# Kernel tuning notes

Measured on AMD Instinct MI355X. Metric: run time of the kernel, lower is better.

## Reference

```python
import jax, jax.numpy as jnp
import numpy as np

H = 128          # hidden_dim
EPS = 1e-5       # BatchNorm eps


def _mean_aggr(h_src, src_idx, dst_idx, num_dst):
    # scatter-mean of h_src rows (gathered by src_idx) onto dst nodes
    msgs = h_src[src_idx]                                   # [E, H] gather
    s = jax.ops.segment_sum(msgs, dst_idx, num_segments=num_dst)
    c = jax.ops.segment_sum(jnp.ones((dst_idx.shape[0],), h_src.dtype),
                            dst_idx, num_segments=num_dst)
    return s / jnp.maximum(c, 1.0)[:, None]


def _bn_eval(h, g, b, m, v):
    return (h - m) * jax.lax.rsqrt(v + EPS) * g + b


def setup_inputs() -> dict:
    key = jax.random.key(0)
    ks = jax.random.split(key, 32)
    Nu, Nr, E, Din, ED = 100000, 100000, 500000, 32, 16
    d = {}
    d['x_user'] = jax.random.normal(ks[0], (Nu, Din), jnp.float32)
    d['x_recipient'] = jax.random.normal(ks[1], (Nr, Din), jnp.float32)
    d['edge_attr'] = jax.random.normal(ks[2], (E, ED), jnp.float32)
    d['edge_index_ut'] = jax.random.randint(ks[3], (2, E), 0, Nr)  # user->recipient
    d['edge_index_ru'] = jax.random.randint(ks[4], (2, E), 0, Nu)  # recipient->user
    sc = 0.05
    # input projections (Linear: y = x @ W + b, W stored [in, out])
    d['proj_uW'] = jax.random.normal(ks[5], (Din, H), jnp.float32) * sc
    d['proj_ub'] = jnp.zeros((H,), jnp.float32)
    d['proj_rW'] = jax.random.normal(ks[6], (Din, H), jnp.float32) * sc
    d['proj_rb'] = jnp.zeros((H,), jnp.float32)
    # SAGEConv params: [num_layers=2, num_edge_types=2, ...]
    d['sage_Wl'] = jax.random.normal(ks[7], (2, 2, H, H), jnp.float32) * sc
    d['sage_bl'] = jnp.zeros((2, 2, H), jnp.float32)
    d['sage_Wr'] = jax.random.normal(ks[8], (2, 2, H, H), jnp.float32) * sc
    # BatchNorm (eval): [num_layers=2, num_node_types=2 (0=user,1=recipient), H]
    d['bn_g'] = jnp.ones((2, 2, H), jnp.float32)
    d['bn_b'] = jnp.zeros((2, 2, H), jnp.float32)
    d['bn_m'] = jax.random.normal(ks[9], (2, 2, H), jnp.float32) * 0.01
    d['bn_v'] = jnp.ones((2, 2, H), jnp.float32)
    # EdgePredictor MLP: (2H + edge_dim) -> H -> H//2 -> 1
    din = 2 * H + ED
    d['ep_W1'] = jax.random.normal(ks[10], (din, H), jnp.float32) * sc
    d['ep_b1'] = jnp.zeros((H,), jnp.float32)
    d['ep_bng'] = jnp.ones((H,), jnp.float32)
    d['ep_bnb'] = jnp.zeros((H,), jnp.float32)
    d['ep_bnm'] = jax.random.normal(ks[11], (H,), jnp.float32) * 0.01
    d['ep_bnv'] = jnp.ones((H,), jnp.float32)
    d['ep_W2'] = jax.random.normal(ks[12], (H, H // 2), jnp.float32) * sc
    d['ep_b2'] = jnp.zeros((H // 2,), jnp.float32)
    d['ep_W3'] = jax.random.normal(ks[13], (H // 2, 1), jnp.float32) * sc
    d['ep_b3'] = jnp.zeros((1,), jnp.float32)
    return d


def reference(x_user, x_recipient, edge_attr, edge_index_ut, edge_index_ru,
              proj_uW, proj_ub, proj_rW, proj_rb,
              sage_Wl, sage_bl, sage_Wr,
              bn_g, bn_b, bn_m, bn_v,
              ep_W1, ep_b1, ep_bng, ep_bnb, ep_bnm, ep_bnv,
              ep_W2, ep_b2, ep_W3, ep_b3):
    Nu = x_user.shape[0]
    Nr = x_recipient.shape[0]
    # input projections
    h_u = x_user @ proj_uW + proj_ub        # [Nu, H]
    h_r = x_recipient @ proj_rW + proj_rb   # [Nr, H]

    for i in range(2):  # num_layers
        # edge type 0: user -> recipient (SAGE mean aggr + root)
        agg_r = _mean_aggr(h_u, edge_index_ut[0], edge_index_ut[1], Nr)
        new_r = agg_r @ sage_Wl[i, 0] + sage_bl[i, 0] + h_r @ sage_Wr[i, 0]
        # edge type 1: recipient -> user
        agg_u = _mean_aggr(h_r, edge_index_ru[0], edge_index_ru[1], Nu)
        new_u = agg_u @ sage_Wl[i, 1] + sage_bl[i, 1] + h_u @ sage_Wr[i, 1]
        # BN (eval) + ReLU (dropout inactive) + residual
        new_u = jax.nn.relu(_bn_eval(new_u, bn_g[i, 0], bn_b[i, 0], bn_m[i, 0], bn_v[i, 0])) + h_u
        new_r = jax.nn.relu(_bn_eval(new_r, bn_g[i, 1], bn_b[i, 1], bn_m[i, 1], bn_v[i, 1])) + h_r
        h_u, h_r = new_u, new_r

    # edge predictor on target edge type (user -> recipient)
    src = h_u[edge_index_ut[0]]   # [E, H]
    dst = h_r[edge_index_ut[1]]   # [E, H]
    x = jnp.concatenate([src, dst, edge_attr], axis=1)  # [E, 2H+ED]
    h = jax.nn.relu(x @ ep_W1 + ep_b1)
    h = _bn_eval(h, ep_bng, ep_bnb, ep_bnm, ep_bnv)
    h = jax.nn.relu(h @ ep_W2 + ep_b2)
    out = jax.nn.sigmoid(h @ ep_W3 + ep_b3)
    return out.squeeze(-1)  # [E]
```

## Files before the change

### kernel.cpp

```cpp
#include <hip/hip_runtime.h>
#include <math.h>

#define H 128
#define BN_EPS 1e-5f

typedef __attribute__((ext_vector_type(8))) short bf16x8;
typedef __attribute__((ext_vector_type(4))) float f32x4;

__device__ __forceinline__ unsigned short f2bf(float f) {
    unsigned int u = __float_as_uint(f);
    u += 0x7fffu + ((u >> 16) & 1u);
    return (unsigned short)(u >> 16);
}
__device__ __forceinline__ float bf2f(unsigned short s) {
    return __uint_as_float(((unsigned int)s) << 16);
}
__device__ __forceinline__ f32x4 mfma16(bf16x8 a, bf16x8 b, f32x4 c) {
    return __builtin_amdgcn_mfma_f32_16x16x32_bf16(a, b, c, 0, 0, 0);
}

__device__ __forceinline__ void wfrag_one(const float* __restrict__ src,
                                          unsigned short* __restrict__ dst,
                                          int K, int N, int idx) {
    int l = idx & 63;
    int rest = idx >> 6;
    int ntn = N >> 4;
    int nt = rest % ntn;
    int kc = rest / ntn;
    int n = nt * 16 + (l & 15);
    int k0 = kc * 32 + (l >> 4) * 8;
    bf16x8 v;
    #pragma unroll
    for (int j = 0; j < 8; ++j) {
        int k = k0 + j;
        v[j] = (short)((k < K) ? f2bf(src[(size_t)k * N + n]) : 0);
    }
    *(bf16x8*)(dst + (size_t)idx * 8) = v;
}

__global__ __launch_bounds__(256)
void wfrag_all(const float* __restrict__ W1, const float* __restrict__ W2,
               const float* __restrict__ pu, const float* __restrict__ pr,
               const float* __restrict__ Wl, const float* __restrict__ Wr,
               unsigned short* __restrict__ W1f, unsigned short* __restrict__ W2f,
               unsigned short* __restrict__ puf, unsigned short* __restrict__ prf,
               unsigned short* __restrict__ sageWf) {
    int bx = blockIdx.x;
    if (bx < 26) {
        int idx = bx * 256 + threadIdx.x;
        if (idx < 4608)      wfrag_one(W1, W1f, 272, 128, idx);
        else if (idx < 5632) wfrag_one(W2, W2f, 128, 64, idx - 4608);
        else if (idx < 6144) wfrag_one(pu, puf, 32, 128, idx - 5632);
        else if (idx < 6656) wfrag_one(pr, prf, 32, 128, idx - 6144);
    } else {
        int idx = (bx - 26) * 256 + threadIdx.x;
        int seg = idx >> 11;
        int sub = idx & 2047;
        int lt = seg >> 1;
        int half = seg & 1;
        const float* src = (half ? Wr : Wl) + (size_t)lt * H * H;
        unsigned short* dst = sageWf + (size_t)lt * 32768 + half * 16384;
        wfrag_one(src, dst, 128, 128, sub);
    }
}

__global__ __launch_bounds__(256)
void proj_kernel(const float* __restrict__ xu, const float* __restrict__ xr,
                 const unsigned short* __restrict__ puf, const float* __restrict__ bu,
                 const unsigned short* __restrict__ prf, const float* __restrict__ br,
                 unsigned short* __restrict__ hub, unsigned short* __restrict__ hrb,
                 int Nu, int Nr, int nbu) {
    int bx = blockIdx.x;
    const float* x; const unsigned short* Wf; const float* bias;
    unsigned short* hb; int N; int row0;
    if (bx < nbu) { x = xu; Wf = puf; bias = bu; hb = hub; N = Nu; row0 = bx * 64; }
    else          { x = xr; Wf = prf; bias = br; hb = hrb; N = Nr; row0 = (bx - nbu) * 64; }

    int tid = threadIdx.x, l = tid & 63, w = tid >> 6, l15 = l & 15, quad = l >> 4;
    int arow = row0 + w * 16 + l15;

    bf16x8 a = {0, 0, 0, 0, 0, 0, 0, 0};
    if (arow < N) {
        const float* xp = x + (size_t)arow * 32 + quad * 8;
        float4 v0 = *(const float4*)xp;
        float4 v1 = *(const float4*)(xp + 4);
        a[0] = (short)f2bf(v0.x); a[1] = (short)f2bf(v0.y);
        a[2] = (short)f2bf(v0.z); a[3] = (short)f2bf(v0.w);
        a[4] = (short)f2bf(v1.x); a[5] = (short)f2bf(v1.y);
        a[6] = (short)f2bf(v1.z); a[7] = (short)f2bf(v1.w);
    }
    f32x4 acc[8];
    #pragma unroll
    for (int nt = 0; nt < 8; ++nt) {
        bf16x8 b = *(const bf16x8*)(Wf + (size_t)(nt * 64 + l) * 8);
        acc[nt] = mfma16(a, b, (f32x4){0.f, 0.f, 0.f, 0.f});
    }
    #pragma unroll
    for (int reg = 0; reg < 4; ++reg) {
        int row = row0 + w * 16 + quad * 4 + reg;
        if (row < N) {
            #pragma unroll
            for (int nt = 0; nt < 8; ++nt) {
                int col = nt * 16 + l15;
                hb[(size_t)row * H + col] = f2bf(acc[nt][reg] + bias[col]);
            }
        }
    }
}

__global__ __launch_bounds__(256)
void hist_kernel(const int* __restrict__ dstR, const int* __restrict__ dstU,
                 int* __restrict__ degR, int* __restrict__ degU, int E, int EB) {
    int bx = blockIdx.x;
    const int* dst = (bx < EB) ? dstR : dstU;
    int* deg = (bx < EB) ? degR : degU;
    int e = ((bx < EB) ? bx : bx - EB) * 256 + threadIdx.x;
    if (e < E) atomicAdd(&deg[dst[e]], 1);
}

__global__ __launch_bounds__(256)
void scan1_kernel(const int* __restrict__ degR, const int* __restrict__ degU,
                  int* __restrict__ partR, int* __restrict__ partU, int Nr, int Nu, int NBr) {
    int bx = blockIdx.x;
    const int* deg = (bx < NBr) ? degR : degU;
    int* part = (bx < NBr) ? partR : partU;
    int lb = (bx < NBr) ? bx : bx - NBr;
    int N = (bx < NBr) ? Nr : Nu;
    __shared__ int s[256];
    int t = threadIdx.x;
    int i = lb * 256 + t;
    s[t] = (i < N) ? deg[i] : 0;
    __syncthreads();
    for (int o = 128; o > 0; o >>= 1) {
        if (t < o) s[t] += s[t + o];
        __syncthreads();
    }
    if (t == 0) part[lb] = s[0];
}

__global__ __launch_bounds__(256)
void scan3_kernel(const int* __restrict__ degR, const int* __restrict__ degU,
                  const int* __restrict__ partR, const int* __restrict__ partU,
                  int* __restrict__ offR, int* __restrict__ offU, int Nr, int Nu, int NBr) {
    int bx = blockIdx.x;
    const int* deg = (bx < NBr) ? degR : degU;
    const int* part = (bx < NBr) ? partR : partU;
    int* off = (bx < NBr) ? offR : offU;
    int lb = (bx < NBr) ? bx : bx - NBr;
    int N = (bx < NBr) ? Nr : Nu;
    __shared__ int s[256];
    __shared__ int ps[256];
    int t = threadIdx.x;

    int pv = 0;
    if (t < lb) pv += part[t];
    if (t + 256 < lb) pv += part[t + 256];
    ps[t] = pv;
    __syncthreads();
    for (int o = 128; o > 0; o >>= 1) {
        if (t < o) ps[t] += ps[t + o];
        __syncthreads();
    }
    int pref = ps[0];

    int i = lb * 256 + t;
    int v = (i < N) ? deg[i] : 0;
    s[t] = v;
    __syncthreads();
    for (int o = 1; o < 256; o <<= 1) {
        int x = (t >= o) ? s[t - o] : 0;
        __syncthreads();
        s[t] += x;
        __syncthreads();
    }
    if (i < N) off[i] = pref + s[t] - v;
    if (i == N - 1) off[N] = pref + s[t];
}

__global__ __launch_bounds__(256)
void fill_kernel(const int* __restrict__ srcR, const int* __restrict__ dstR,
                 const int* __restrict__ srcU, const int* __restrict__ dstU,
                 const int* __restrict__ offR, const int* __restrict__ offU,
                 int* __restrict__ degR, int* __restrict__ degU,
                 int* __restrict__ eidR, int* __restrict__ eidU,
                 int* __restrict__ epermR, int* __restrict__ epdstR,
                 int E, int EB) {
    int bx = blockIdx.x;
    bool isR = bx < EB;
    const int* src = isR ? srcR : srcU;
    const int* dst = isR ? dstR : dstU;
    const int* off = isR ? offR : offU;
    int* deg = isR ? degR : degU;
    int* eid = isR ? eidR : eidU;
    int e = (isR ? bx : bx - EB) * 256 + threadIdx.x;
    if (e < E) {
        int d = dst[e];
        int p = off[d] + atomicSub(&deg[d], 1) - 1;
        eid[p] = src[e];
        if (isR) {
            epermR[p] = e;
            epdstR[p] = d;
        }
    }
}

__global__ __launch_bounds__(256)
void layer_kernel(const unsigned short* __restrict__ hu_o, const unsigned short* __restrict__ hr_o,
                  unsigned short* __restrict__ hu_n, unsigned short* __restrict__ hr_n,
                  const int* __restrict__ off_r, const int* __restrict__ eid_r,
                  const int* __restrict__ off_u, const int* __restrict__ eid_u,
                  int Nu, int Nr, int nbr,
                  const unsigned short* __restrict__ WfR, const float* __restrict__ blR,
                  const float* __restrict__ gR, const float* __restrict__ bR,
                  const float* __restrict__ mR, const float* __restrict__ vR,
                  const unsigned short* __restrict__ WfU, const float* __restrict__ blU,
                  const float* __restrict__ gU, const float* __restrict__ bU,
                  const float* __restrict__ mU, const float* __restrict__ vU) {
    int bx = blockIdx.x;
    const unsigned short* gsrc; const unsigned short* own; unsigned short* outp;
    const int* off; const int* eid; const unsigned short* Wf;
    const float *bl, *bg, *bb, *bm, *bv;
    int N, row0;
    if (bx < nbr) {
        gsrc = hu_o; own = hr_o; outp = hr_n; off = off_r; eid = eid_r;
        Wf = WfR; bl = blR; bg = gR; bb = bR; bm = mR; bv = vR;
        N = Nr; row0 = bx * 64;
    } else {
        gsrc = hr_o; own = hu_o; outp = hu_n; off = off_u; eid = eid_u;
        Wf = WfU; bl = blU; bg = gU; bb = bU; bm = mU; bv = vU;
        N = Nu; row0 = (bx - nbr) * 64;
    }

    __shared__ float sc[128], sh[128], bias[128];
    __shared__ int perm[64];
    int tid = threadIdx.x;
    if (tid < 128) {
        float s = bg[tid] * rsqrtf(bv[tid] + BN_EPS);
        sc[tid] = s;
        sh[tid] = bb[tid] - bm[tid] * s;
        bias[tid] = bl[tid];
    }
    if (tid < 64) {
        int rr = row0 + tid;
        int dg = (rr < N) ? (off[rr + 1] - off[rr]) : 0;
        int key = (min(dg, 255) << 8) | tid;
        for (int k = 2; k <= 64; k <<= 1) {
            for (int j = k >> 1; j > 0; j >>= 1) {
                int p = __shfl_xor(key, j);
                bool keepmin = (((tid & j) == 0) == ((tid & k) == 0));
                key = keepmin ? (key < p ? key : p) : (key > p ? key : p);
            }
        }
        perm[tid] = key & 255;
    }
    __syncthreads();

    int l = tid & 63, w = tid >> 6, l15 = l & 15, quad = l >> 4;
    int rloc = perm[w * 16 + l15];
    int arow = row0 + rloc;
    bool rok = (arow < N);
    size_t rbase = (size_t)(rok ? arow : 0) * H;
    int s0 = rok ? off[arow] : 0;
    int s1 = rok ? off[arow + 1] : 0;

    bf16x8 ownfr[4];
    #pragma unroll
    for (int kc = 0; kc < 4; ++kc)
        ownfr[kc] = *(const bf16x8*)(own + rbase + kc * 32 + quad * 8);

    float ag[4][8];
    #pragma unroll
    for (int kc = 0; kc < 4; ++kc)
        #pragma unroll
        for (int j = 0; j < 8; ++j) ag[kc][j] = 0.0f;

    for (int i = s0; i < s1; ++i) {
        int s = eid[i];
        const unsigned short* rp = gsrc + (size_t)s * H + quad * 8;
        #pragma unroll
        for (int kc = 0; kc < 4; ++kc) {
            bf16x8 v = *(const bf16x8*)(rp + kc * 32);
            #pragma unroll
            for (int j = 0; j < 8; ++j) ag[kc][j] += bf2f((unsigned short)v[j]);
        }
    }
    float inv = (s1 > s0) ? 1.0f / (float)(s1 - s0) : 0.0f;

    f32x4 acc[8];
    #pragma unroll
    for (int nt = 0; nt < 8; ++nt) acc[nt] = (f32x4){0.f, 0.f, 0.f, 0.f};

    #pragma unroll
    for (int kc = 0; kc < 4; ++kc) {
        bf16x8 a;
        #pragma unroll
        for (int j = 0; j < 8; ++j) a[j] = (short)f2bf(ag[kc][j] * inv);
        #pragma unroll
        for (int nt = 0; nt < 8; ++nt) {
            bf16x8 b = *(const bf16x8*)(Wf + (size_t)((kc * 8 + nt) * 64 + l) * 8);
            acc[nt] = mfma16(a, b, acc[nt]);
        }
    }
    #pragma unroll
    for (int kc = 4; kc < 8; ++kc) {
        #pragma unroll
        for (int nt = 0; nt < 8; ++nt) {
            bf16x8 b = *(const bf16x8*)(Wf + (size_t)((kc * 8 + nt) * 64 + l) * 8);
            acc[nt] = mfma16(ownfr[kc - 4], b, acc[nt]);
        }
    }

    #pragma unroll
    for (int reg = 0; reg < 4; ++reg) {
        int crow = row0 + perm[w * 16 + quad * 4 + reg];
        if (crow < N) {
            #pragma unroll
            for (int nt = 0; nt < 8; ++nt) {
                int col = nt * 16 + l15;
                float g = acc[nt][reg] + bias[col];
                g = g * sc[col] + sh[col];
                float hv = bf2f(own[(size_t)crow * H + col]);
                outp[(size_t)crow * H + col] = f2bf(fmaxf(g, 0.0f) + hv);
            }
        }
    }
}

__global__ __launch_bounds__(256)
void ep_kernel(const unsigned short* __restrict__ hub, const unsigned short* __restrict__ hrb,
               const float* __restrict__ ea,
               const int* __restrict__ slot_src, const int* __restrict__ slot_dst,
               const int* __restrict__ slot_eid,
               const unsigned short* __restrict__ W1f, const float* __restrict__ b1,
               const float* __restrict__ bng, const float* __restrict__ bnb,
               const float* __restrict__ bnm, const float* __restrict__ bnv,
               const unsigned short* __restrict__ W2f, const float* __restrict__ b2,
               const float* __restrict__ W3, const float* __restrict__ b3,
               float* __restrict__ out, int E) {
    __shared__ unsigned short h1s[64][136];
    __shared__ int se[64], de[64], pe[64];
    __shared__ float sc1[128], sh1[128], bi1[128];

    int tid = threadIdx.x;
    int p0 = blockIdx.x * 64;
    if (tid < 64) {
        int p = p0 + tid;
        bool v = (p < E);
        se[tid] = v ? slot_src[p] : 0;
        de[tid] = v ? slot_dst[p] : 0;
        pe[tid] = v ? slot_eid[p] : 0;
    }
    if (tid < 128) {
        float s = bng[tid] * rsqrtf(bnv[tid] + BN_EPS);
        sc1[tid] = s;
        sh1[tid] = bnb[tid] - bnm[tid] * s;
        bi1[tid] = b1[tid];
    }
    __syncthreads();

    int l = tid & 63, w = tid >> 6, l15 = l & 15, quad = l >> 4;
    int arow = w * 16 + l15;
    size_t soff = (size_t)se[arow] * H;
    size_t doff = (size_t)de[arow] * H;
    int eorig = pe[arow];
    bool ev = (p0 + arow < E);

    bf16x8 afr[9];
    #pragma unroll
    for (int kc = 0; kc < 4; ++kc)
        afr[kc] = *(const bf16x8*)(hub + soff + kc * 32 + quad * 8);
    #pragma unroll
    for (int kc = 0; kc < 4; ++kc)
        afr[4 + kc] = *(const bf16x8*)(hrb + doff + kc * 32 + quad * 8);
    {
        bf16x8 a = {0, 0, 0, 0, 0, 0, 0, 0};
        if (quad < 2 && ev) {
            const float* p = ea + (size_t)eorig * 16 + quad * 8;
            float4 v0 = *(const float4*)p;
            float4 v1 = *(const float4*)(p + 4);
            a[0] = (short)f2bf(v0.x); a[1] = (short)f2bf(v0.y);
            a[2] = (short)f2bf(v0.z); a[3] = (short)f2bf(v0.w);
            a[4] = (short)f2bf(v1.x); a[5] = (short)f2bf(v1.y);
            a[6] = (short)f2bf(v1.z); a[7] = (short)f2bf(v1.w);
        }
        afr[8] = a;
    }

    f32x4 acc[8];
    #pragma unroll
    for (int nt = 0; nt < 8; ++nt) acc[nt] = (f32x4){0.f, 0.f, 0.f, 0.f};

    #pragma unroll
    for (int kc = 0; kc < 9; ++kc) {
        #pragma unroll
        for (int nt = 0; nt < 8; ++nt) {
            bf16x8 b = *(const bf16x8*)(W1f + (size_t)((kc * 8 + nt) * 64 + l) * 8);
            acc[nt] = mfma16(afr[kc], b, acc[nt]);
        }
    }

    #pragma unroll
    for (int nt = 0; nt < 8; ++nt) {
        #pragma unroll
        for (int reg = 0; reg < 4; ++reg) {
            int row = w * 16 + quad * 4 + reg;
            int col = nt * 16 + l15;
            float z = acc[nt][reg] + bi1[col];
            z = fmaxf(z, 0.0f);
            z = z * sc1[col] + sh1[col];
            h1s[row][col] = f2bf(z);
        }
    }
    __syncthreads();

    f32x4 acc2[4];
    #pragma unroll
    for (int nt = 0; nt < 4; ++nt) acc2[nt] = (f32x4){0.f, 0.f, 0.f, 0.f};
    #pragma unroll
    for (int kc = 0; kc < 4; ++kc) {
        bf16x8 a2 = *(const bf16x8*)&h1s[w * 16 + l15][kc * 32 + quad * 8];
        #pragma unroll
        for (int nt = 0; nt < 4; ++nt) {
            bf16x8 b = *(const bf16x8*)(W2f + (size_t)((kc * 4 + nt) * 64 + l) * 8);
            acc2[nt] = mfma16(a2, b, acc2[nt]);
        }
    }

    float part[4] = {0.f, 0.f, 0.f, 0.f};
    #pragma unroll
    for (int nt = 0; nt < 4; ++nt) {
        int col = nt * 16 + l15;
        float w3v = W3[col];
        float b2v = b2[col];
        #pragma unroll
        for (int reg = 0; reg < 4; ++reg)
            part[reg] += fmaxf(acc2[nt][reg] + b2v, 0.0f) * w3v;
    }
    #pragma unroll
    for (int m = 1; m < 16; m <<= 1) {
        #pragma unroll
        for (int reg = 0; reg < 4; ++reg)
            part[reg] += __shfl_xor(part[reg], m);
    }
    if (l15 < 4) {
        int row = w * 16 + quad * 4 + l15;
        if (p0 + row < E) {
            int eo = pe[row];
            out[eo] = 1.0f / (1.0f + expf(-(part[l15] + b3[0])));
        }
    }
}

extern "C" void kernel_launch(void* const* d_in, const int* in_sizes, int n_in,
                              void* d_out, int out_size, void* d_ws, size_t ws_size,
                              hipStream_t stream) {
    const float* x_u     = (const float*)d_in[0];
    const float* x_r     = (const float*)d_in[1];
    const float* eattr   = (const float*)d_in[2];
    const int*   ei_ut   = (const int*)d_in[3];
    const int*   ei_ru   = (const int*)d_in[4];
    const float* proj_uW = (const float*)d_in[5];
    const float* proj_ub = (const float*)d_in[6];
    const float* proj_rW = (const float*)d_in[7];
    const float* proj_rb = (const float*)d_in[8];
    const float* sage_Wl = (const float*)d_in[9];
    const float* sage_bl = (const float*)d_in[10];
    const float* sage_Wr = (const float*)d_in[11];
    const float* bn_g    = (const float*)d_in[12];
    const float* bn_b    = (const float*)d_in[13];
    const float* bn_m    = (const float*)d_in[14];
    const float* bn_v    = (const float*)d_in[15];
    const float* ep_W1   = (const float*)d_in[16];
    const float* ep_b1   = (const float*)d_in[17];
    const float* ep_bng  = (const float*)d_in[18];
    const float* ep_bnb  = (const float*)d_in[19];
    const float* ep_bnm  = (const float*)d_in[20];
    const float* ep_bnv  = (const float*)d_in[21];
    const float* ep_W2   = (const float*)d_in[22];
    const float* ep_b2   = (const float*)d_in[23];
    const float* ep_W3   = (const float*)d_in[24];
    const float* ep_b3   = (const float*)d_in[25];

    int Nu = in_sizes[0] / 32;
    int Nr = in_sizes[1] / 32;
    int E  = in_sizes[3] / 2;

    unsigned short* us = (unsigned short*)d_ws;
    unsigned short* h0_u = us;   us += (size_t)Nu * H;
    unsigned short* h0_r = us;   us += (size_t)Nr * H;
    unsigned short* h1_u = us;   us += (size_t)Nu * H;
    unsigned short* h1_r = us;   us += (size_t)Nr * H;
    unsigned short* W1f  = us;   us += 36864;
    unsigned short* W2f  = us;   us += 8192;
    unsigned short* puf  = us;   us += 4096;
    unsigned short* prf  = us;   us += 4096;
    unsigned short* sageWf = us; us += 131072;
    int* ip     = (int*)us;
    int* off_r  = ip;  ip += Nr + 1;
    int* off_u  = ip;  ip += Nu + 1;
    int* deg_r  = ip;  ip += Nr;
    int* deg_u  = ip;  ip += Nu;
    int* eid_r  = ip;  ip += E;
    int* eid_u  = ip;  ip += E;
    int* eperm_r = ip; ip += E;
    int* epdst_r = ip; ip += E;
    int* part_r = ip;  ip += 512;
    int* part_u = ip;  ip += 512;

    const int* ut_src = ei_ut;
    const int* ut_dst = ei_ut + E;
    const int* ru_src = ei_ru;
    const int* ru_dst = ei_ru + E;

    int EB  = (E + 255) / 256;
    int NBr = (Nr + 255) / 256;
    int NBu = (Nu + 255) / 256;

    wfrag_all<<<90, 256, 0, stream>>>(ep_W1, ep_W2, proj_uW, proj_rW,
                                      sage_Wl, sage_Wr,
                                      W1f, W2f, puf, prf, sageWf);

    hipMemsetAsync(deg_r, 0, (size_t)(Nr + Nu) * sizeof(int), stream);
    hist_kernel<<<2 * EB, 256, 0, stream>>>(ut_dst, ru_dst, deg_r, deg_u, E, EB);
    scan1_kernel<<<NBr + NBu, 256, 0, stream>>>(deg_r, deg_u, part_r, part_u, Nr, Nu, NBr);
    scan3_kernel<<<NBr + NBu, 256, 0, stream>>>(deg_r, deg_u, part_r, part_u,
                                                off_r, off_u, Nr, Nu, NBr);
    fill_kernel<<<2 * EB, 256, 0, stream>>>(ut_src, ut_dst, ru_src, ru_dst,
                                            off_r, off_u, deg_r, deg_u,
                                            eid_r, eid_u, eperm_r, epdst_r, E, EB);

    int nbu = (Nu + 63) / 64, nbr = (Nr + 63) / 64;
    proj_kernel<<<nbu + nbr, 256, 0, stream>>>(x_u, x_r, puf, proj_ub, prf, proj_rb,
                                               h0_u, h0_r, Nu, Nr, nbu);

    for (int layer = 0; layer < 2; ++layer) {
        const unsigned short* iu = (layer == 0) ? h0_u : h1_u;
        const unsigned short* ir = (layer == 0) ? h0_r : h1_r;
        unsigned short* ou = (layer == 0) ? h1_u : h0_u;
        unsigned short* orr = (layer == 0) ? h1_r : h0_r;

        const unsigned short* Wf0 = sageWf + ((size_t)layer * 2 + 0) * 32768;
        const unsigned short* Wf1 = sageWf + ((size_t)layer * 2 + 1) * 32768;
        const float* bl0 = sage_bl + ((size_t)layer * 2 + 0) * H;
        const float* bl1 = sage_bl + ((size_t)layer * 2 + 1) * H;
        const float* g0 = bn_g + ((size_t)layer * 2 + 0) * H;
        const float* b0 = bn_b + ((size_t)layer * 2 + 0) * H;
        const float* m0 = bn_m + ((size_t)layer * 2 + 0) * H;
        const float* v0 = bn_v + ((size_t)layer * 2 + 0) * H;
        const float* g1 = bn_g + ((size_t)layer * 2 + 1) * H;
        const float* b1 = bn_b + ((size_t)layer * 2 + 1) * H;
        const float* m1 = bn_m + ((size_t)layer * 2 + 1) * H;
        const float* v1 = bn_v + ((size_t)layer * 2 + 1) * H;

        layer_kernel<<<nbr + nbu, 256, 0, stream>>>(
            iu, ir, ou, orr,
            off_r, eid_r, off_u, eid_u,
            Nu, Nr, nbr,
            Wf0, bl0, g1, b1, m1, v1,
            Wf1, bl1, g0, b0, m0, v0);
    }

    ep_kernel<<<(E + 63) / 64, 256, 0, stream>>>(h0_u, h0_r, eattr,
                                                 eid_r, epdst_r, eperm_r,
                                                 W1f, ep_b1,
                                                 ep_bng, ep_bnb, ep_bnm, ep_bnv,
                                                 W2f, ep_b2, ep_W3, ep_b3,
                                                 (float*)d_out, E);
}
```

Baseline: 553.8 us.

## Keep an FP8 shadow copy of node features for gathers in layers and edge predictor

Proj and layer kernels now also write an FP8 (swizzled) copy of each node's hidden vector next to the bf16 one. The mean-aggregation gathers and the edge-predictor gathers read these 128-byte FP8 rows instead of 256-byte bf16 rows, cutting random-gather traffic in half. This costs an extra scattered byte store per element, conversion work, and a large loss of precision in the aggregated messages and edge-predictor inputs.

```diff
diff --git a/kernel.cpp b/kernel.cpp
--- a/kernel.cpp
+++ b/kernel.cpp
@@ -6,6 +6,7 @@
 
 typedef __attribute__((ext_vector_type(8))) short bf16x8;
 typedef __attribute__((ext_vector_type(4))) float f32x4;
+typedef __attribute__((ext_vector_type(2))) float f32x2;
 
 __device__ __forceinline__ unsigned short f2bf(float f) {
     unsigned int u = __float_as_uint(f);
@@ -17,6 +18,10 @@
 }
 __device__ __forceinline__ f32x4 mfma16(bf16x8 a, bf16x8 b, f32x4 c) {
     return __builtin_amdgcn_mfma_f32_16x16x32_bf16(a, b, c, 0, 0, 0);
+}
+__device__ __forceinline__ unsigned char f2fp8(float f) {
+    int p = __builtin_amdgcn_cvt_pk_fp8_f32(f, f, 0, false);
+    return (unsigned char)(p & 0xff);
 }
 
 __device__ __forceinline__ void wfrag_one(const float* __restrict__ src,
@@ -64,17 +69,25 @@
     }
 }
 
+__device__ __forceinline__ int swz_of(int col) {
+    int kc = col >> 5;
+    int q = (col >> 3) & 3;
+    int j = col & 7;
+    return q * 32 + kc * 8 + j;
+}
+
 __global__ __launch_bounds__(256)
 void proj_kernel(const float* __restrict__ xu, const float* __restrict__ xr,
                  const unsigned short* __restrict__ puf, const float* __restrict__ bu,
                  const unsigned short* __restrict__ prf, const float* __restrict__ br,
                  unsigned short* __restrict__ hub, unsigned short* __restrict__ hrb,
+                 unsigned char* __restrict__ h8u, unsigned char* __restrict__ h8r,
                  int Nu, int Nr, int nbu) {
     int bx = blockIdx.x;
     const float* x; const unsigned short* Wf; const float* bias;
-    unsigned short* hb; int N; int row0;
-    if (bx < nbu) { x = xu; Wf = puf; bias = bu; hb = hub; N = Nu; row0 = bx * 64; }
-    else          { x = xr; Wf = prf; bias = br; hb = hrb; N = Nr; row0 = (bx - nbu) * 64; }
+    unsigned short* hb; unsigned char* h8; int N; int row0;
+    if (bx < nbu) { x = xu; Wf = puf; bias = bu; hb = hub; h8 = h8u; N = Nu; row0 = bx * 64; }
+    else          { x = xr; Wf = prf; bias = br; hb = hrb; h8 = h8r; N = Nr; row0 = (bx - nbu) * 64; }
 
     int tid = threadIdx.x, l = tid & 63, w = tid >> 6, l15 = l & 15, quad = l >> 4;
     int arow = row0 + w * 16 + l15;
@@ -102,7 +115,9 @@
             #pragma unroll
             for (int nt = 0; nt < 8; ++nt) {
                 int col = nt * 16 + l15;
-                hb[(size_t)row * H + col] = f2bf(acc[nt][reg] + bias[col]);
+                float v = acc[nt][reg] + bias[col];
+                hb[(size_t)row * H + col] = f2bf(v);
+                h8[(size_t)row * H + swz_of(col)] = f2fp8(v);
             }
         }
     }
@@ -206,7 +221,9 @@
 
 __global__ __launch_bounds__(256)
 void layer_kernel(const unsigned short* __restrict__ hu_o, const unsigned short* __restrict__ hr_o,
+                  const unsigned char* __restrict__ h8u_o, const unsigned char* __restrict__ h8r_o,
                   unsigned short* __restrict__ hu_n, unsigned short* __restrict__ hr_n,
+                  unsigned char* __restrict__ h8u_n, unsigned char* __restrict__ h8r_n,
                   const int* __restrict__ off_r, const int* __restrict__ eid_r,
                   const int* __restrict__ off_u, const int* __restrict__ eid_u,
                   int Nu, int Nr, int nbr,
@@ -217,16 +234,16 @@
                   const float* __restrict__ gU, const float* __restrict__ bU,
                   const float* __restrict__ mU, const float* __restrict__ vU) {
     int bx = blockIdx.x;
-    const unsigned short* gsrc; const unsigned short* own; unsigned short* outp;
+    const unsigned short* own; const unsigned char* g8; unsigned short* outp; unsigned char* out8;
     const int* off; const int* eid; const unsigned short* Wf;
     const float *bl, *bg, *bb, *bm, *bv;
     int N, row0;
     if (bx < nbr) {
-        gsrc = hu_o; own = hr_o; outp = hr_n; off = off_r; eid = eid_r;
+        g8 = h8u_o; own = hr_o; outp = hr_n; out8 = h8r_n; off = off_r; eid = eid_r;
         Wf = WfR; bl = blR; bg = gR; bb = bR; bm = mR; bv = vR;
         N = Nr; row0 = bx * 64;
     } else {
-        gsrc = hr_o; own = hu_o; outp = hu_n; off = off_u; eid = eid_u;
+        g8 = h8r_o; own = hu_o; outp = hu_n; out8 = h8u_n; off = off_u; eid = eid_u;
         Wf = WfU; bl = blU; bg = gU; bb = bU; bm = mU; bv = vU;
         N = Nu; row0 = (bx - nbr) * 64;
     }
@@ -276,13 +293,17 @@
 
     for (int i = s0; i < s1; ++i) {
         int s = eid[i];
-        const unsigned short* rp = gsrc + (size_t)s * H + quad * 8;
-        #pragma unroll
-        for (int kc = 0; kc < 4; ++kc) {
-            bf16x8 v = *(const bf16x8*)(rp + kc * 32);
-            #pragma unroll
-            for (int j = 0; j < 8; ++j) ag[kc][j] += bf2f((unsigned short)v[j]);
-        }
+        const uint4* rp = (const uint4*)(g8 + (size_t)s * H + quad * 32);
+        uint4 w0 = rp[0];
+        uint4 w1 = rp[1];
+        #define ACC4(word, kc, jb) { \
+            f32x2 lo_ = __builtin_amdgcn_cvt_pk_f32_fp8((int)(word), false); \
+            f32x2 hi_ = __builtin_amdgcn_cvt_pk_f32_fp8((int)(word), true);  \
+            ag[kc][jb + 0] += lo_[0]; ag[kc][jb + 1] += lo_[1]; \
+            ag[kc][jb + 2] += hi_[0]; ag[kc][jb + 3] += hi_[1]; }
+        ACC4(w0.x, 0, 0) ACC4(w0.y, 0, 4) ACC4(w0.z, 1, 0) ACC4(w0.w, 1, 4)
+        ACC4(w1.x, 2, 0) ACC4(w1.y, 2, 4) ACC4(w1.z, 3, 0) ACC4(w1.w, 3, 4)
+        #undef ACC4
     }
     float inv = (s1 > s0) ? 1.0f / (float)(s1 - s0) : 0.0f;
 
@@ -320,14 +341,29 @@
                 float g = acc[nt][reg] + bias[col];
                 g = g * sc[col] + sh[col];
                 float hv = bf2f(own[(size_t)crow * H + col]);
-                outp[(size_t)crow * H + col] = f2bf(fmaxf(g, 0.0f) + hv);
+                float o = fmaxf(g, 0.0f) + hv;
+                outp[(size_t)crow * H + col] = f2bf(o);
+                out8[(size_t)crow * H + swz_of(col)] = f2fp8(o);
             }
         }
     }
 }
 
-__global__ __launch_bounds__(256)
-void ep_kernel(const unsigned short* __restrict__ hub, const unsigned short* __restrict__ hrb,
+__device__ __forceinline__ bf16x8 frag_fp8pair(unsigned int wa, unsigned int wb) {
+    f32x2 a0 = __builtin_amdgcn_cvt_pk_f32_fp8((int)wa, false);
+    f32x2 a1 = __builtin_amdgcn_cvt_pk_f32_fp8((int)wa, true);
+    f32x2 b0 = __builtin_amdgcn_cvt_pk_f32_fp8((int)wb, false);
+    f32x2 b1 = __builtin_amdgcn_cvt_pk_f32_fp8((int)wb, true);
+    bf16x8 r;
+    r[0] = (short)f2bf(a0[0]); r[1] = (short)f2bf(a0[1]);
+    r[2] = (short)f2bf(a1[0]); r[3] = (short)f2bf(a1[1]);
+    r[4] = (short)f2bf(b0[0]); r[5] = (short)f2bf(b0[1]);
+    r[6] = (short)f2bf(b1[0]); r[7] = (short)f2bf(b1[1]);
+    return r;
+}
+
+__global__ __launch_bounds__(256)
+void ep_kernel(const unsigned char* __restrict__ h8u, const unsigned char* __restrict__ h8r,
                const float* __restrict__ ea,
                const int* __restrict__ slot_src, const int* __restrict__ slot_dst,
                const int* __restrict__ slot_eid,
@@ -360,31 +396,33 @@
 
     int l = tid & 63, w = tid >> 6, l15 = l & 15, quad = l >> 4;
     int arow = w * 16 + l15;
-    size_t soff = (size_t)se[arow] * H;
-    size_t doff = (size_t)de[arow] * H;
     int eorig = pe[arow];
     bool ev = (p0 + arow < E);
 
+    const uint4* sp = (const uint4*)(h8u + (size_t)se[arow] * H + quad * 32);
+    const uint4* dp = (const uint4*)(h8r + (size_t)de[arow] * H + quad * 32);
+    uint4 sw0 = sp[0], sw1 = sp[1];
+    uint4 dw0 = dp[0], dw1 = dp[1];
+    bf16x8 aea = {0, 0, 0, 0, 0, 0, 0, 0};
+    if (quad < 2 && ev) {
+        const float* p = ea + (size_t)eorig * 16 + quad * 8;
+        float4 v0 = *(const float4*)p;
+        float4 v1 = *(const float4*)(p + 4);
+        aea[0] = (short)f2bf(v0.x); aea[1] = (short)f2bf(v0.y);
+        aea[2] = (short)f2bf(v0.z); aea[3] = (short)f2bf(v0.w);
+        aea[4] = (short)f2bf(v1.x); aea[5] = (short)f2bf(v1.y);
+        aea[6] = (short)f2bf(v1.z); aea[7] = (short)f2bf(v1.w);
+    }
     bf16x8 afr[9];
-    #pragma unroll
-    for (int kc = 0; kc < 4; ++kc)
-        afr[kc] = *(const bf16x8*)(hub + soff + kc * 32 + quad * 8);
-    #pragma unroll
-    for (int kc = 0; kc < 4; ++kc)
-        afr[4 + kc] = *(const bf16x8*)(hrb + doff + kc * 32 + quad * 8);
-    {
-        bf16x8 a = {0, 0, 0, 0, 0, 0, 0, 0};
-        if (quad < 2 && ev) {
-            const float* p = ea + (size_t)eorig * 16 + quad * 8;
-            float4 v0 = *(const float4*)p;
-            float4 v1 = *(const float4*)(p + 4);
-            a[0] = (short)f2bf(v0.x); a[1] = (short)f2bf(v0.y);
-            a[2] = (short)f2bf(v0.z); a[3] = (short)f2bf(v0.w);
-            a[4] = (short)f2bf(v1.x); a[5] = (short)f2bf(v1.y);
-            a[6] = (short)f2bf(v1.z); a[7] = (short)f2bf(v1.w);
-        }
-        afr[8] = a;
-    }
+    afr[0] = frag_fp8pair(sw0.x, sw0.y);
+    afr[1] = frag_fp8pair(sw0.z, sw0.w);
+    afr[2] = frag_fp8pair(sw1.x, sw1.y);
+    afr[3] = frag_fp8pair(sw1.z, sw1.w);
+    afr[4] = frag_fp8pair(dw0.x, dw0.y);
+    afr[5] = frag_fp8pair(dw0.z, dw0.w);
+    afr[6] = frag_fp8pair(dw1.x, dw1.y);
+    afr[7] = frag_fp8pair(dw1.z, dw1.w);
+    afr[8] = aea;
 
     f32x4 acc[8];
     #pragma unroll
@@ -495,7 +533,11 @@
     unsigned short* puf  = us;   us += 4096;
     unsigned short* prf  = us;   us += 4096;
     unsigned short* sageWf = us; us += 131072;
-    int* ip     = (int*)us;
+    unsigned char* f80_u = (unsigned char*)us;
+    unsigned char* f80_r = f80_u + (size_t)Nu * H;
+    unsigned char* f81_u = f80_r + (size_t)Nr * H;
+    unsigned char* f81_r = f81_u + (size_t)Nu * H;
+    int* ip     = (int*)(f81_r + (size_t)Nr * H);
     int* off_r  = ip;  ip += Nr + 1;
     int* off_u  = ip;  ip += Nu + 1;
     int* deg_r  = ip;  ip += Nr;
@@ -531,13 +573,17 @@
 
     int nbu = (Nu + 63) / 64, nbr = (Nr + 63) / 64;
     proj_kernel<<<nbu + nbr, 256, 0, stream>>>(x_u, x_r, puf, proj_ub, prf, proj_rb,
-                                               h0_u, h0_r, Nu, Nr, nbu);
+                                               h0_u, h0_r, f80_u, f80_r, Nu, Nr, nbu);
 
     for (int layer = 0; layer < 2; ++layer) {
         const unsigned short* iu = (layer == 0) ? h0_u : h1_u;
         const unsigned short* ir = (layer == 0) ? h0_r : h1_r;
+        const unsigned char* i8u = (layer == 0) ? f80_u : f81_u;
+        const unsigned char* i8r = (layer == 0) ? f80_r : f81_r;
         unsigned short* ou = (layer == 0) ? h1_u : h0_u;
         unsigned short* orr = (layer == 0) ? h1_r : h0_r;
+        unsigned char* o8u = (layer == 0) ? f81_u : f80_u;
+        unsigned char* o8r = (layer == 0) ? f81_r : f80_r;
 
         const unsigned short* Wf0 = sageWf + ((size_t)layer * 2 + 0) * 32768;
         const unsigned short* Wf1 = sageWf + ((size_t)layer * 2 + 1) * 32768;
@@ -553,14 +599,14 @@
         const float* v1 = bn_v + ((size_t)layer * 2 + 1) * H;
 
         layer_kernel<<<nbr + nbu, 256, 0, stream>>>(
-            iu, ir, ou, orr,
+            iu, ir, i8u, i8r, ou, orr, o8u, o8r,
             off_r, eid_r, off_u, eid_u,
             Nu, Nr, nbr,
             Wf0, bl0, g1, b1, m1, v1,
             Wf1, bl1, g0, b0, m0, v0);
     }
 
-    ep_kernel<<<(E + 63) / 64, 256, 0, stream>>>(h0_u, h0_r, eattr,
+    ep_kernel<<<(E + 63) / 64, 256, 0, stream>>>(f80_u, f80_r, eattr,
                                                  eid_r, epdst_r, eperm_r,
                                                  W1f, ep_b1,
                                                  ep_bng, ep_bnb, ep_bnm, ep_bnv,
```

Measured after the change: 550.4 us. About the same (-0.6%).
